# Performance work log

Measured on AMD Instinct MI355X. Metric: run time of the kernel, lower is better.

Reference implementation:

```python
import jax, jax.numpy as jnp
import numpy as np

B, T, C, HS = 4, 2048, 1024, 128

def setup_inputs() -> dict:
    key = jax.random.key(0)
    k0, k1, k2, k3 = jax.random.split(key, 4)
    scale = 1.0 / np.sqrt(C)
    return {
        "x": jax.random.normal(k0, (B, T, C), dtype=jnp.float32),
        "Wk": jax.random.normal(k1, (C, HS), dtype=jnp.float32) * scale,
        "Wq": jax.random.normal(k2, (C, HS), dtype=jnp.float32) * scale,
        "Wv": jax.random.normal(k3, (C, HS), dtype=jnp.float32) * scale,
    }

def reference(x, Wk, Wq, Wv):
    # k, q, v: [B, T, HS]
    k = jnp.einsum('btc,ch->bth', x, Wk)
    q = jnp.einsum('btc,ch->bth', x, Wq)
    v = jnp.einsum('btc,ch->bth', x, Wv)
    hs = k.shape[-1]
    # full T x T scores (no causal mask in source), scaled by head_size**-0.5
    wei = jnp.einsum('bqh,bkh->bqk', q, k) * (hs ** -0.5)
    wei = jax.nn.softmax(wei, axis=-1)
    # dropout p=0.0 -> identity
    out = jnp.einsum('bqk,bkh->bqh', wei, v)
    return out
```

## Files before the change

### kernel.cpp

```cpp
#include <hip/hip_runtime.h>
#include <hip/hip_bf16.h>

typedef float  f32x4  __attribute__((ext_vector_type(4)));
typedef float  f32x8  __attribute__((ext_vector_type(8)));
typedef float  f32x16 __attribute__((ext_vector_type(16)));
typedef short  s8v    __attribute__((ext_vector_type(8)));
typedef __bf16 b8v    __attribute__((ext_vector_type(8)));
typedef unsigned int u32;
typedef unsigned short ushort;

#define T_DIM  2048
#define C_DIM  1024


typedef const __attribute__((address_space(1))) u32 gu32;
typedef __attribute__((address_space(3))) u32 lu32;

static __device__ __forceinline__ void glds16(const void* g, void* l) {
  __builtin_amdgcn_global_load_lds((gu32*)g, (lu32*)l, 16, 0, 0);
}

static __device__ __forceinline__ b8v ldb8(const ushort* p) {
  return __builtin_bit_cast(b8v, *reinterpret_cast<const s8v*>(p));
}

static __device__ __forceinline__ b8v cvt8(f32x8 v) {
  b8v r;
#pragma unroll
  for (int i = 0; i < 8; ++i) r[i] = (__bf16)v[i];
  return r;
}

static __device__ __forceinline__ ushort bfu(float f) {
  __bf16 h = (__bf16)f;
  return __builtin_bit_cast(ushort, h);
}

static __device__ __forceinline__ f32x4 mfma16(b8v a, b8v b, f32x4 c) {
  return __builtin_amdgcn_mfma_f32_16x16x32_bf16(a, b, c, 0, 0, 0);
}

static __device__ __forceinline__ f32x16 mfma32(b8v a, b8v b, f32x16 c) {
  return __builtin_amdgcn_mfma_f32_32x32x16_bf16(a, b, c, 0, 0, 0);
}

#define BAR_VM(N)                                                        \
  asm volatile("s_waitcnt vmcnt(" #N ") lgkmcnt(0)" ::: "memory");       \
  __builtin_amdgcn_s_barrier();                                          \
  asm volatile("" ::: "memory");

__global__ __launch_bounds__(256) void wconv(const float* __restrict__ Wq,
                                             const float* __restrict__ Wk,
                                             const float* __restrict__ Wv,
                                             ushort* __restrict__ Wt) {
  __shared__ float lds[64][65];
  const int m  = blockIdx.z;
  const int c0 = blockIdx.x * 64;
  const int h0 = blockIdx.y * 64;
  const float* W = (m == 0) ? Wq : (m == 1) ? Wk : Wv;

  const int cl = threadIdx.x >> 4;
  const int h4 = (threadIdx.x & 15) * 4;
#pragma unroll
  for (int i = 0; i < 4; ++i) {
    int c = cl + i * 16;
    float4 v = *reinterpret_cast<const float4*>(W + (c0 + c) * 128 + h0 + h4);
    lds[c][h4] = v.x; lds[c][h4 + 1] = v.y;
    lds[c][h4 + 2] = v.z; lds[c][h4 + 3] = v.w;
  }
  __syncthreads();
  const int hl = threadIdx.x >> 2;
  const int cs = (threadIdx.x & 3) * 16;
  s8v o0, o1;
#pragma unroll
  for (int i = 0; i < 8; ++i) o0[i] = (short)bfu(lds[cs + i][hl]);
#pragma unroll
  for (int i = 0; i < 8; ++i) o1[i] = (short)bfu(lds[cs + 8 + i][hl]);
  ushort* dst = Wt + (m * 128 + h0 + hl) * C_DIM + c0 + cs;
  *reinterpret_cast<s8v*>(dst) = o0;
  *reinterpret_cast<s8v*>(dst + 8) = o1;
}

__global__ __launch_bounds__(256) void proj(const float* __restrict__ x,
                                            const ushort* __restrict__ Wt,
                                            ushort* __restrict__ q,
                                            ushort* __restrict__ k,
                                            ushort* __restrict__ vt) {
  __shared__ __align__(16) ushort Ab[2][32 * 72];
  __shared__ __align__(16) ushort Bb[2][128 * 64];
  __shared__ __align__(16) ushort stage[5120];

  const int t   = threadIdx.x;
  const int w   = t >> 6;
  const int lid = t & 63;
  const int lr  = lid & 15;
  const int g   = lid >> 4;
  const int wr  = w >> 1;
  const int wc  = w & 1;
  const int m   = blockIdx.y;
  const int r0  = blockIdx.x * 32;

  const int arow = t >> 3;
  const int acol = (t & 7) * 8;
  const float* ag = x + (r0 + arow) * C_DIM + acol;

  const int bswz = (((lid & 7) ^ (lid >> 3)) << 4);
  const char* bg = (const char*)(Wt + m * 128 * C_DIM);

  f32x4 acc[4] = {};

#pragma unroll
  for (int j = 0; j < 4; ++j) {
    int h = j * 32 + w * 8 + (lid >> 3);
    glds16(bg + h * 2048 + bswz, (char*)&Bb[0][0] + j * 4096 + w * 1024);
  }
  {
    f32x8 av = *reinterpret_cast<const f32x8*>(ag);
    b8v ac = cvt8(av);
    *reinterpret_cast<s8v*>(&Ab[0][arow * 72 + acol]) =
        __builtin_bit_cast(s8v, ac);
  }
  __syncthreads();

  int cur = 0;
#pragma unroll 1
  for (int i = 0; i < 16; ++i) {
    const int nxt = cur ^ 1;
    f32x8 an;
    if (i < 15) {
      const int kk = (i + 1) * 64;
#pragma unroll
      for (int j = 0; j < 4; ++j) {
        int h = j * 32 + w * 8 + (lid >> 3);
        glds16(bg + h * 2048 + kk * 2 + bswz,
               (char*)&Bb[nxt][0] + j * 4096 + w * 1024);
      }
      an = *reinterpret_cast<const f32x8*>(ag + kk);
    }

#pragma unroll
    for (int kk2 = 0; kk2 < 2; ++kk2) {
      b8v af = ldb8(&Ab[cur][(wr * 16 + lr) * 72 + kk2 * 32 + g * 8]);
#pragma unroll
      for (int cn = 0; cn < 4; ++cn) {
        int h = wc * 64 + cn * 16 + lr;
        int inner = (kk2 * 64 + g * 16) ^ ((h & 7) << 4);
        b8v bf = ldb8(
            (const ushort*)((const char*)&Bb[cur][h * 64] + inner));
        acc[cn] = mfma16(af, bf, acc[cn]);
      }
    }

    if (i < 15) {
      b8v anc = cvt8(an);
      *reinterpret_cast<s8v*>(&Ab[nxt][arow * 72 + acol]) =
          __builtin_bit_cast(s8v, anc);
    }
    __syncthreads();
    cur = nxt;
  }

  if (m < 2) {
#pragma unroll
    for (int cn = 0; cn < 4; ++cn)
#pragma unroll
      for (int j = 0; j < 4; ++j)
        stage[(wr * 16 + 4 * g + j) * 136 + wc * 64 + cn * 16 + lr] =
            bfu(acc[cn][j]);
    __syncthreads();
    ushort* dst = (m == 0) ? q : k;
#pragma unroll
    for (int c = 0; c < 2; ++c) {
      int chunk = c * 256 + t;
      int row = chunk >> 4, col8 = chunk & 15;
      s8v v8 = *reinterpret_cast<const s8v*>(&stage[row * 136 + col8 * 8]);
      *reinterpret_cast<s8v*>(&dst[(r0 + row) * 128 + col8 * 8]) = v8;
    }
  } else {
#pragma unroll
    for (int cn = 0; cn < 4; ++cn)
#pragma unroll
      for (int j = 0; j < 4; ++j)
        stage[(wc * 64 + cn * 16 + lr) * 40 + wr * 16 + 4 * g + j] =
            bfu(acc[cn][j]);
    __syncthreads();
    int b = blockIdx.x >> 6;
    int tbase = (blockIdx.x & 63) * 32;
#pragma unroll
    for (int c = 0; c < 2; ++c) {
      int chunk = c * 256 + t;
      int h = chunk >> 2, t8 = chunk & 3;
      s8v v8 = *reinterpret_cast<const s8v*>(&stage[h * 40 + t8 * 8]);
      *reinterpret_cast<s8v*>(&vt[(b * 128 + h) * T_DIM + tbase + t8 * 8]) = v8;
    }
  }
}

__global__ __launch_bounds__(512) void attn(const ushort* __restrict__ q,
                                            const ushort* __restrict__ k,
                                            const ushort* __restrict__ vt,
                                            float* __restrict__ out,
                                            float* __restrict__ opart,
                                            float* __restrict__ lp0,
                                            float* __restrict__ lp1) {
  extern __shared__ __align__(16) char smem[];

  const int t   = threadIdx.x;
  const int w   = t >> 6;
  const int lid = t & 63;
  const int hi  = lid >> 5;
  const int ln  = lid & 31;
  const int wq  = w >> 2;
  const int wk  = w & 3;
  const int b   = blockIdx.y;
  const int z   = blockIdx.z;
  const int t0  = blockIdx.x * 64;

  const ushort* qp = q + (b * T_DIM + t0 + wq * 32) * 128;
  b8v aq[8];
#pragma unroll
  for (int s = 0; s < 8; ++s)
    aq[s] = ldb8(&qp[ln * 128 + s * 16 + hi * 8]);

  const char* kgb = (const char*)(k + b * T_DIM * 128);
  const char* vgb = (const char*)(vt + b * 128 * T_DIM);
  const int kv_base = z * 1024;

  const int R = wk * 32 + ln;
  int koff[8];
#pragma unroll
  for (int s = 0; s < 8; ++s)
    koff[s] = R * 256 + (((s * 2 + hi) ^ (R & 15)) << 4);
  int voff[4][2];
#pragma unroll
  for (int ht = 0; ht < 4; ++ht)
#pragma unroll
    for (int s = 0; s < 2; ++s) {
      int Hrow = ht * 32 + ln;
      int chunk = wk * 4 + s * 2 + hi;
      voff[ht][s] = 32768 + Hrow * 256 + ((chunk ^ (Hrow & 15)) << 4);
    }

  f32x16 of[4] = {};
  float lsum = 0.0f;
  const float scale = 0.08838834764831845f;

#define ATTN_STAGE(KV0, BUF)                                              \
  _Pragma("unroll") for (int j = 0; j < 4; ++j) {                         \
    int row = w * 16 + j * 4 + (lid >> 4);                                \
    int p_ = (row >> 2) & 7;                                              \
    int pg = (p_ & 4) | ((p_ & 1) << 1) | ((p_ >> 1) & 1);                \
    int srow = (row & ~31) | (pg << 2) | (row & 3);                       \
    glds16(kgb + ((KV0) + srow) * 256 + (((lid & 15) ^ (row & 15)) << 4), \
           smem + (BUF) * 65536 + w * 4096 + j * 1024);                   \
  }                                                                       \
  _Pragma("unroll") for (int j = 0; j < 4; ++j) {                         \
    int h = w * 16 + j * 4 + (lid >> 4);                                  \
    glds16(vgb + h * 4096 + (KV0) * 2 + (((lid & 15) ^ (h & 15)) << 4),   \
           smem + (BUF) * 65536 + 32768 + w * 4096 + j * 1024);           \
  }

#define ATTN_BODY(BUF)                                                   \
  {                                                                      \
    const char* Tb = smem + (BUF) * 65536;                               \
    b8v kfr[8];                                                          \
    _Pragma("unroll") for (int s = 0; s < 8; ++s)                        \
        kfr[s] = ldb8((const ushort*)(Tb + koff[s]));                    \
    f32x16 S = {};                                                       \
    __builtin_amdgcn_s_setprio(1);                                       \
    _Pragma("unroll") for (int s = 0; s < 8; ++s)                        \
        S = mfma32(kfr[s], aq[s], S);                                    \
    __builtin_amdgcn_s_setprio(0);                                       \
    float p[16];                                                         \
    _Pragma("unroll") for (int r = 0; r < 16; ++r) {                     \
      p[r] = __expf(S[r] * scale - 4.0f);                                \
      lsum += p[r];                                                      \
    }                                                                    \
    b8v pk0, pk1;                                                        \
    _Pragma("unroll") for (int r = 0; r < 8; ++r) {                      \
      pk0[r] = (__bf16)p[r];                                             \
      pk1[r] = (__bf16)p[8 + r];                                         \
    }                                                                    \
    __builtin_amdgcn_s_setprio(1);                                       \
    _Pragma("unroll") for (int ht = 0; ht < 4; ++ht) {                   \
      b8v v0 = ldb8((const ushort*)(Tb + voff[ht][0]));                  \
      b8v v1 = ldb8((const ushort*)(Tb + voff[ht][1]));                  \
      of[ht] = mfma32(pk0, v0, of[ht]);                                  \
      of[ht] = mfma32(pk1, v1, of[ht]);                                  \
    }                                                                    \
    __builtin_amdgcn_s_setprio(0);                                       \
  }

  ATTN_STAGE(kv_base, 0)

#pragma unroll 1
  for (int i = 0; i < 8; ++i) {
    BAR_VM(0)
    if (i < 7) { ATTN_STAGE(kv_base + (i + 1) * 128, (i + 1) & 1) }
    ATTN_BODY(i & 1)
  }

#undef ATTN_STAGE
#undef ATTN_BODY

  lsum += __shfl_xor(lsum, 32);

  __syncthreads();

  float* ob = (float*)smem;
  float* lb = (float*)(smem + 98304);

  if (lid < 32) lb[(wq * 4 + wk) * 32 + lid] = lsum;
  if (wk != 0) {
#pragma unroll
    for (int ht = 0; ht < 4; ++ht)
#pragma unroll
      for (int r = 0; r < 16; ++r) {
        int qm = (r & 3) + 8 * (r >> 2) + 4 * hi;
        ob[((wk - 1) * 64 + wq * 32 + qm) * 128 + ht * 32 + ln] = of[ht][r];
      }
  }
  __syncthreads();
  if (wk == 0) {
    float* dsto = (z == 0) ? out : opart;
#pragma unroll
    for (int ht = 0; ht < 4; ++ht)
#pragma unroll
      for (int r = 0; r < 16; ++r) {
        int qm = (r & 3) + 8 * (r >> 2) + 4 * hi;
        int row = wq * 32 + qm;
        int col = ht * 32 + ln;
        float val = of[ht][r] + ob[(0 * 64 + row) * 128 + col] +
                    ob[(1 * 64 + row) * 128 + col] +
                    ob[(2 * 64 + row) * 128 + col];
        dsto[(b * T_DIM + t0 + row) * 128 + col] = val;
      }
    if (lid < 32) {
      float lt = lb[(wq * 4 + 0) * 32 + lid] + lb[(wq * 4 + 1) * 32 + lid] +
                 lb[(wq * 4 + 2) * 32 + lid] + lb[(wq * 4 + 3) * 32 + lid];
      float* lp = (z == 0) ? lp0 : lp1;
      lp[b * T_DIM + t0 + wq * 32 + lid] = lt;
    }
  }
}

__global__ __launch_bounds__(256) void fin(float* __restrict__ out,
                                           const float* __restrict__ opart,
                                           const float* __restrict__ lp0,
                                           const float* __restrict__ lp1) {
  int tid = blockIdx.x * 256 + threadIdx.x;
  int idx = tid * 4;
  int row = idx >> 7;
  float inv = 1.0f / (lp0[row] + lp1[row]);
  f32x4 a = *reinterpret_cast<const f32x4*>(out + idx);
  f32x4 c = *reinterpret_cast<const f32x4*>(opart + idx);
  f32x4 r;
#pragma unroll
  for (int i = 0; i < 4; ++i) r[i] = (a[i] + c[i]) * inv;
  *reinterpret_cast<f32x4*>(out + idx) = r;
}

extern "C" void kernel_launch(void* const* d_in, const int* in_sizes, int n_in,
                              void* d_out, int out_size, void* d_ws,
                              size_t ws_size, hipStream_t stream) {
  const float* x  = (const float*)d_in[0];
  const float* Wk = (const float*)d_in[1];
  const float* Wq = (const float*)d_in[2];
  const float* Wv = (const float*)d_in[3];
  float* out = (float*)d_out;

  char* ws = (char*)d_ws;
  ushort* Wt  = (ushort*)ws;
  ushort* qb  = (ushort*)(ws + (1u << 20));
  ushort* kb  = (ushort*)(ws + 3u * (1u << 20));
  ushort* vtb = (ushort*)(ws + 5u * (1u << 20));
  float* opart = (float*)(ws + 8u * (1u << 20));
  float* lp0   = (float*)(ws + 12u * (1u << 20));
  float* lp1   = lp0 + 8192;

  (void)hipFuncSetAttribute(reinterpret_cast<const void*>(&attn),
                            hipFuncAttributeMaxDynamicSharedMemorySize, 131072);

  wconv<<<dim3(16, 2, 3), dim3(256), 0, stream>>>(Wq, Wk, Wv, Wt);
  proj<<<dim3(256, 3), dim3(256), 0, stream>>>(x, Wt, qb, kb, vtb);
  attn<<<dim3(32, 4, 2), dim3(512), 131072, stream>>>(qb, kb, vtb, out, opart,
                                                      lp0, lp1);
  fin<<<dim3(1024), dim3(256), 0, stream>>>(out, opart, lp0, lp1);
}
```

Before: 48.83 us.

## Enlarge projection row tile to 64 and switch to 32x32x16 MFMA

The projection kernel now handles 64 rows of x per block instead of 32, halving the grid and reusing each staged weight tile across twice as many rows. The inner product moves from 16x16x32 to 32x32x16 bf16 MFMAs, with two interleaved accumulators per column tile that are summed at the end, and s_setprio is raised around the MFMA bursts. The epilogue staging is redone for the new accumulator layout. This cuts weight-tile reloads and LDS reads per FLOP, at the cost of fewer blocks (384) and more registers and LDS per block.

Result: slower. 51.90 us (+6.3%).

```diff
diff --git a/kernel.cpp b/kernel.cpp
--- a/kernel.cpp
+++ b/kernel.cpp
@@ -34,10 +34,6 @@
 static __device__ __forceinline__ ushort bfu(float f) {
   __bf16 h = (__bf16)f;
   return __builtin_bit_cast(ushort, h);
-}
-
-static __device__ __forceinline__ f32x4 mfma16(b8v a, b8v b, f32x4 c) {
-  return __builtin_amdgcn_mfma_f32_16x16x32_bf16(a, b, c, 0, 0, 0);
 }
 
 static __device__ __forceinline__ f32x16 mfma32(b8v a, b8v b, f32x16 c) {
@@ -86,39 +82,45 @@
                                             ushort* __restrict__ q,
                                             ushort* __restrict__ k,
                                             ushort* __restrict__ vt) {
-  __shared__ __align__(16) ushort Ab[2][32 * 72];
+  __shared__ __align__(16) ushort Ab[2][64 * 72];
   __shared__ __align__(16) ushort Bb[2][128 * 64];
-  __shared__ __align__(16) ushort stage[5120];
+  __shared__ __align__(16) ushort stage[128 * 72];
 
   const int t   = threadIdx.x;
   const int w   = t >> 6;
   const int lid = t & 63;
-  const int lr  = lid & 15;
-  const int g   = lid >> 4;
-  const int wr  = w >> 1;
-  const int wc  = w & 1;
+  const int hi  = lid >> 5;
+  const int ln  = lid & 31;
+  const int mr  = w >> 1;
+  const int nc  = w & 1;
   const int m   = blockIdx.y;
-  const int r0  = blockIdx.x * 32;
-
-  const int arow = t >> 3;
-  const int acol = (t & 7) * 8;
+  const int r0  = blockIdx.x * 64;
+
+  const int arow = t >> 2;
+  const int acol = (t & 3) * 16;
   const float* ag = x + (r0 + arow) * C_DIM + acol;
 
   const int bswz = (((lid & 7) ^ (lid >> 3)) << 4);
   const char* bg = (const char*)(Wt + m * 128 * C_DIM);
 
-  f32x4 acc[4] = {};
-
-#pragma unroll
-  for (int j = 0; j < 4; ++j) {
-    int h = j * 32 + w * 8 + (lid >> 3);
-    glds16(bg + h * 2048 + bswz, (char*)&Bb[0][0] + j * 4096 + w * 1024);
-  }
+  f32x16 acc[2][2] = {};
+
+#define PROJ_BSTAGE(KK, BUF)                                              \
+  _Pragma("unroll") for (int j = 0; j < 4; ++j) {                         \
+    int h = j * 32 + w * 8 + (lid >> 3);                                  \
+    glds16(bg + h * 2048 + (KK) * 2 + bswz,                               \
+           (char*)&Bb[BUF][0] + j * 4096 + w * 1024);                     \
+  }
+
+  f32x8 a0 = *reinterpret_cast<const f32x8*>(ag);
+  f32x8 a1 = *reinterpret_cast<const f32x8*>(ag + 8);
+  PROJ_BSTAGE(0, 0)
   {
-    f32x8 av = *reinterpret_cast<const f32x8*>(ag);
-    b8v ac = cvt8(av);
+    b8v c0 = cvt8(a0), c1 = cvt8(a1);
     *reinterpret_cast<s8v*>(&Ab[0][arow * 72 + acol]) =
-        __builtin_bit_cast(s8v, ac);
+        __builtin_bit_cast(s8v, c0);
+    *reinterpret_cast<s8v*>(&Ab[0][arow * 72 + acol + 8]) =
+        __builtin_bit_cast(s8v, c1);
   }
   __syncthreads();
 
@@ -126,51 +128,57 @@
 #pragma unroll 1
   for (int i = 0; i < 16; ++i) {
     const int nxt = cur ^ 1;
-    f32x8 an;
     if (i < 15) {
       const int kk = (i + 1) * 64;
-#pragma unroll
-      for (int j = 0; j < 4; ++j) {
-        int h = j * 32 + w * 8 + (lid >> 3);
-        glds16(bg + h * 2048 + kk * 2 + bswz,
-               (char*)&Bb[nxt][0] + j * 4096 + w * 1024);
-      }
-      an = *reinterpret_cast<const f32x8*>(ag + kk);
-    }
-
-#pragma unroll
-    for (int kk2 = 0; kk2 < 2; ++kk2) {
-      b8v af = ldb8(&Ab[cur][(wr * 16 + lr) * 72 + kk2 * 32 + g * 8]);
-#pragma unroll
-      for (int cn = 0; cn < 4; ++cn) {
-        int h = wc * 64 + cn * 16 + lr;
-        int inner = (kk2 * 64 + g * 16) ^ ((h & 7) << 4);
+      PROJ_BSTAGE(kk, nxt)
+      a0 = *reinterpret_cast<const f32x8*>(ag + kk);
+      a1 = *reinterpret_cast<const f32x8*>(ag + kk + 8);
+    }
+
+#pragma unroll
+    for (int s = 0; s < 4; ++s) {
+      b8v af = ldb8(&Ab[cur][(mr * 32 + ln) * 72 + s * 16 + hi * 8]);
+      __builtin_amdgcn_s_setprio(1);
+#pragma unroll
+      for (int ct = 0; ct < 2; ++ct) {
+        int h = nc * 64 + ct * 32 + ln;
+        int inner = ((s * 2 + hi) << 4) ^ ((h & 7) << 4);
         b8v bf = ldb8(
             (const ushort*)((const char*)&Bb[cur][h * 64] + inner));
-        acc[cn] = mfma16(af, bf, acc[cn]);
-      }
+        acc[ct][s & 1] = mfma32(af, bf, acc[ct][s & 1]);
+      }
+      __builtin_amdgcn_s_setprio(0);
     }
 
     if (i < 15) {
-      b8v anc = cvt8(an);
+      b8v c0 = cvt8(a0), c1 = cvt8(a1);
       *reinterpret_cast<s8v*>(&Ab[nxt][arow * 72 + acol]) =
-          __builtin_bit_cast(s8v, anc);
+          __builtin_bit_cast(s8v, c0);
+      *reinterpret_cast<s8v*>(&Ab[nxt][arow * 72 + acol + 8]) =
+          __builtin_bit_cast(s8v, c1);
     }
     __syncthreads();
     cur = nxt;
   }
+#undef PROJ_BSTAGE
+
+  f32x16 fa[2];
+#pragma unroll
+  for (int ct = 0; ct < 2; ++ct) fa[ct] = acc[ct][0] + acc[ct][1];
 
   if (m < 2) {
 #pragma unroll
-    for (int cn = 0; cn < 4; ++cn)
-#pragma unroll
-      for (int j = 0; j < 4; ++j)
-        stage[(wr * 16 + 4 * g + j) * 136 + wc * 64 + cn * 16 + lr] =
-            bfu(acc[cn][j]);
+    for (int ct = 0; ct < 2; ++ct)
+#pragma unroll
+      for (int r = 0; r < 16; ++r) {
+        int row = mr * 32 + (r & 3) + 8 * (r >> 2) + 4 * hi;
+        int col = nc * 64 + ct * 32 + ln;
+        stage[row * 136 + col] = bfu(fa[ct][r]);
+      }
     __syncthreads();
     ushort* dst = (m == 0) ? q : k;
 #pragma unroll
-    for (int c = 0; c < 2; ++c) {
+    for (int c = 0; c < 4; ++c) {
       int chunk = c * 256 + t;
       int row = chunk >> 4, col8 = chunk & 15;
       s8v v8 = *reinterpret_cast<const s8v*>(&stage[row * 136 + col8 * 8]);
@@ -178,20 +186,22 @@
     }
   } else {
 #pragma unroll
-    for (int cn = 0; cn < 4; ++cn)
-#pragma unroll
-      for (int j = 0; j < 4; ++j)
-        stage[(wc * 64 + cn * 16 + lr) * 40 + wr * 16 + 4 * g + j] =
-            bfu(acc[cn][j]);
+    for (int ct = 0; ct < 2; ++ct)
+#pragma unroll
+      for (int r = 0; r < 16; ++r) {
+        int trow = mr * 32 + (r & 3) + 8 * (r >> 2) + 4 * hi;
+        int h = nc * 64 + ct * 32 + ln;
+        stage[h * 72 + trow] = bfu(fa[ct][r]);
+      }
     __syncthreads();
-    int b = blockIdx.x >> 6;
-    int tbase = (blockIdx.x & 63) * 32;
-#pragma unroll
-    for (int c = 0; c < 2; ++c) {
+    int bb = blockIdx.x >> 5;
+    int tbase = (blockIdx.x & 31) * 64;
+#pragma unroll
+    for (int c = 0; c < 4; ++c) {
       int chunk = c * 256 + t;
-      int h = chunk >> 2, t8 = chunk & 3;
-      s8v v8 = *reinterpret_cast<const s8v*>(&stage[h * 40 + t8 * 8]);
-      *reinterpret_cast<s8v*>(&vt[(b * 128 + h) * T_DIM + tbase + t8 * 8]) = v8;
+      int h = chunk >> 3, t8 = chunk & 7;
+      s8v v8 = *reinterpret_cast<const s8v*>(&stage[h * 72 + t8 * 8]);
+      *reinterpret_cast<s8v*>(&vt[(bb * 128 + h) * T_DIM + tbase + t8 * 8]) = v8;
     }
   }
 }
@@ -382,7 +392,7 @@
                             hipFuncAttributeMaxDynamicSharedMemorySize, 131072);
 
   wconv<<<dim3(16, 2, 3), dim3(256), 0, stream>>>(Wq, Wk, Wv, Wt);
-  proj<<<dim3(256, 3), dim3(256), 0, stream>>>(x, Wt, qb, kb, vtb);
+  proj<<<dim3(128, 3), dim3(256), 0, stream>>>(x, Wt, qb, kb, vtb);
   attn<<<dim3(32, 4, 2), dim3(512), 131072, stream>>>(qb, kb, vtb, out, opart,
                                                       lp0, lp1);
   fin<<<dim3(1024), dim3(256), 0, stream>>>(out, opart, lp0, lp1);
```

## Add 4-way KV split attention kernel with 128-query tiles when workspace allows

Applied to the files above, without the earlier changes.

Adds an attn4 kernel that processes 128 query rows per block, using 8 waves arranged as 4 query groups by 2 KV halves. Each staged K/V tile is reused across twice as many queries, and the KV sequence is split 4 ways (grid 16x4x4), which keeps 256 blocks. The finalize kernel is generalized to sum nz partial outputs and row sums. This path is selected only when the workspace is at least 21 MiB; otherwise the original 2-way kernel runs. The cost is more partial-output traffic in the finalize step and a dependence on the workspace size.

Result: no change. 48.87 us (+0.1%).

```diff
diff --git a/kernel.cpp b/kernel.cpp
--- a/kernel.cpp
+++ b/kernel.cpp
@@ -195,55 +195,6 @@
     }
   }
 }
-
-__global__ __launch_bounds__(512) void attn(const ushort* __restrict__ q,
-                                            const ushort* __restrict__ k,
-                                            const ushort* __restrict__ vt,
-                                            float* __restrict__ out,
-                                            float* __restrict__ opart,
-                                            float* __restrict__ lp0,
-                                            float* __restrict__ lp1) {
-  extern __shared__ __align__(16) char smem[];
-
-  const int t   = threadIdx.x;
-  const int w   = t >> 6;
-  const int lid = t & 63;
-  const int hi  = lid >> 5;
-  const int ln  = lid & 31;
-  const int wq  = w >> 2;
-  const int wk  = w & 3;
-  const int b   = blockIdx.y;
-  const int z   = blockIdx.z;
-  const int t0  = blockIdx.x * 64;
-
-  const ushort* qp = q + (b * T_DIM + t0 + wq * 32) * 128;
-  b8v aq[8];
-#pragma unroll
-  for (int s = 0; s < 8; ++s)
-    aq[s] = ldb8(&qp[ln * 128 + s * 16 + hi * 8]);
-
-  const char* kgb = (const char*)(k + b * T_DIM * 128);
-  const char* vgb = (const char*)(vt + b * 128 * T_DIM);
-  const int kv_base = z * 1024;
-
-  const int R = wk * 32 + ln;
-  int koff[8];
-#pragma unroll
-  for (int s = 0; s < 8; ++s)
-    koff[s] = R * 256 + (((s * 2 + hi) ^ (R & 15)) << 4);
-  int voff[4][2];
-#pragma unroll
-  for (int ht = 0; ht < 4; ++ht)
-#pragma unroll
-    for (int s = 0; s < 2; ++s) {
-      int Hrow = ht * 32 + ln;
-      int chunk = wk * 4 + s * 2 + hi;
-      voff[ht][s] = 32768 + Hrow * 256 + ((chunk ^ (Hrow & 15)) << 4);
-    }
-
-  f32x16 of[4] = {};
-  float lsum = 0.0f;
-  const float scale = 0.08838834764831845f;
 
 #define ATTN_STAGE(KV0, BUF)                                              \
   _Pragma("unroll") for (int j = 0; j < 4; ++j) {                         \
@@ -260,7 +211,55 @@
            smem + (BUF) * 65536 + 32768 + w * 4096 + j * 1024);           \
   }
 
-#define ATTN_BODY(BUF)                                                   \
+__global__ __launch_bounds__(512) void attn2(const ushort* __restrict__ q,
+                                             const ushort* __restrict__ k,
+                                             const ushort* __restrict__ vt,
+                                             float* __restrict__ out,
+                                             float* __restrict__ parts,
+                                             float* __restrict__ lps) {
+  extern __shared__ __align__(16) char smem[];
+
+  const int t   = threadIdx.x;
+  const int w   = t >> 6;
+  const int lid = t & 63;
+  const int hi  = lid >> 5;
+  const int ln  = lid & 31;
+  const int wq  = w >> 2;
+  const int wk  = w & 3;
+  const int b   = blockIdx.y;
+  const int z   = blockIdx.z;
+  const int t0  = blockIdx.x * 64;
+
+  const ushort* qp = q + (b * T_DIM + t0 + wq * 32) * 128;
+  b8v aq[8];
+#pragma unroll
+  for (int s = 0; s < 8; ++s)
+    aq[s] = ldb8(&qp[ln * 128 + s * 16 + hi * 8]);
+
+  const char* kgb = (const char*)(k + b * T_DIM * 128);
+  const char* vgb = (const char*)(vt + b * 128 * T_DIM);
+  const int kv_base = z * 1024;
+
+  const int R = wk * 32 + ln;
+  int koff[8];
+#pragma unroll
+  for (int s = 0; s < 8; ++s)
+    koff[s] = R * 256 + (((s * 2 + hi) ^ (R & 15)) << 4);
+  int voff[4][2];
+#pragma unroll
+  for (int ht = 0; ht < 4; ++ht)
+#pragma unroll
+    for (int s = 0; s < 2; ++s) {
+      int Hrow = ht * 32 + ln;
+      int chunk = wk * 4 + s * 2 + hi;
+      voff[ht][s] = 32768 + Hrow * 256 + ((chunk ^ (Hrow & 15)) << 4);
+    }
+
+  f32x16 of[4] = {};
+  float lsum = 0.0f;
+  const float scale = 0.08838834764831845f;
+
+#define ATTN2_BODY(BUF)                                                  \
   {                                                                      \
     const char* Tb = smem + (BUF) * 65536;                               \
     b8v kfr[8];                                                          \
@@ -297,11 +296,9 @@
   for (int i = 0; i < 8; ++i) {
     BAR_VM(0)
     if (i < 7) { ATTN_STAGE(kv_base + (i + 1) * 128, (i + 1) & 1) }
-    ATTN_BODY(i & 1)
-  }
-
-#undef ATTN_STAGE
-#undef ATTN_BODY
+    ATTN2_BODY(i & 1)
+  }
+#undef ATTN2_BODY
 
   lsum += __shfl_xor(lsum, 32);
 
@@ -322,7 +319,7 @@
   }
   __syncthreads();
   if (wk == 0) {
-    float* dsto = (z == 0) ? out : opart;
+    float* dsto = (z == 0) ? out : parts;
 #pragma unroll
     for (int ht = 0; ht < 4; ++ht)
 #pragma unroll
@@ -338,25 +335,161 @@
     if (lid < 32) {
       float lt = lb[(wq * 4 + 0) * 32 + lid] + lb[(wq * 4 + 1) * 32 + lid] +
                  lb[(wq * 4 + 2) * 32 + lid] + lb[(wq * 4 + 3) * 32 + lid];
-      float* lp = (z == 0) ? lp0 : lp1;
-      lp[b * T_DIM + t0 + wq * 32 + lid] = lt;
+      lps[z * 8192 + b * T_DIM + t0 + wq * 32 + lid] = lt;
+    }
+  }
+}
+
+__global__ __launch_bounds__(512) void attn4(const ushort* __restrict__ q,
+                                             const ushort* __restrict__ k,
+                                             const ushort* __restrict__ vt,
+                                             float* __restrict__ out,
+                                             float* __restrict__ parts,
+                                             float* __restrict__ lps) {
+  extern __shared__ __align__(16) char smem[];
+
+  const int t   = threadIdx.x;
+  const int w   = t >> 6;
+  const int lid = t & 63;
+  const int hi  = lid >> 5;
+  const int ln  = lid & 31;
+  const int wq  = w >> 1;
+  const int wk  = w & 1;
+  const int b   = blockIdx.y;
+  const int z   = blockIdx.z;
+  const int t0  = blockIdx.x * 128;
+
+  const ushort* qp = q + (b * T_DIM + t0 + wq * 32) * 128;
+  b8v aq[8];
+#pragma unroll
+  for (int s = 0; s < 8; ++s)
+    aq[s] = ldb8(&qp[ln * 128 + s * 16 + hi * 8]);
+
+  const char* kgb = (const char*)(k + b * T_DIM * 128);
+  const char* vgb = (const char*)(vt + b * 128 * T_DIM);
+  const int kv_base = z * 512;
+
+  int koff[2][8];
+#pragma unroll
+  for (int tt = 0; tt < 2; ++tt) {
+    int R = wk * 64 + tt * 32 + ln;
+#pragma unroll
+    for (int s = 0; s < 8; ++s)
+      koff[tt][s] = R * 256 + (((s * 2 + hi) ^ (R & 15)) << 4);
+  }
+  int voff[2][4][2];
+#pragma unroll
+  for (int tt = 0; tt < 2; ++tt)
+#pragma unroll
+    for (int ht = 0; ht < 4; ++ht)
+#pragma unroll
+      for (int s = 0; s < 2; ++s) {
+        int Hrow = ht * 32 + ln;
+        int chunk = wk * 8 + tt * 4 + s * 2 + hi;
+        voff[tt][ht][s] = 32768 + Hrow * 256 + ((chunk ^ (Hrow & 15)) << 4);
+      }
+
+  f32x16 of[4] = {};
+  float lsum = 0.0f;
+  const float scale = 0.08838834764831845f;
+
+#define ATTN4_HALF(TB, TT)                                               \
+  {                                                                      \
+    b8v kfr[8];                                                          \
+    _Pragma("unroll") for (int s = 0; s < 8; ++s)                        \
+        kfr[s] = ldb8((const ushort*)((TB) + koff[TT][s]));              \
+    f32x16 S = {};                                                       \
+    __builtin_amdgcn_s_setprio(1);                                       \
+    _Pragma("unroll") for (int s = 0; s < 8; ++s)                        \
+        S = mfma32(kfr[s], aq[s], S);                                    \
+    __builtin_amdgcn_s_setprio(0);                                       \
+    float p[16];                                                         \
+    _Pragma("unroll") for (int r = 0; r < 16; ++r) {                     \
+      p[r] = __expf(S[r] * scale - 4.0f);                                \
+      lsum += p[r];                                                      \
+    }                                                                    \
+    b8v pk0, pk1;                                                        \
+    _Pragma("unroll") for (int r = 0; r < 8; ++r) {                      \
+      pk0[r] = (__bf16)p[r];                                             \
+      pk1[r] = (__bf16)p[8 + r];                                         \
+    }                                                                    \
+    __builtin_amdgcn_s_setprio(1);                                       \
+    _Pragma("unroll") for (int ht = 0; ht < 4; ++ht) {                   \
+      b8v v0 = ldb8((const ushort*)((TB) + voff[TT][ht][0]));            \
+      b8v v1 = ldb8((const ushort*)((TB) + voff[TT][ht][1]));            \
+      of[ht] = mfma32(pk0, v0, of[ht]);                                  \
+      of[ht] = mfma32(pk1, v1, of[ht]);                                  \
+    }                                                                    \
+    __builtin_amdgcn_s_setprio(0);                                       \
+  }
+
+  ATTN_STAGE(kv_base, 0)
+
+#pragma unroll 1
+  for (int i = 0; i < 4; ++i) {
+    BAR_VM(0)
+    if (i < 3) { ATTN_STAGE(kv_base + (i + 1) * 128, (i + 1) & 1) }
+    const char* Tb = smem + (i & 1) * 65536;
+    ATTN4_HALF(Tb, 0)
+    ATTN4_HALF(Tb, 1)
+  }
+#undef ATTN4_HALF
+
+  lsum += __shfl_xor(lsum, 32);
+
+  __syncthreads();
+
+  float* ob = (float*)smem;
+  float* lb = (float*)(smem + 65536);
+
+  if (lid < 32) lb[(wk * 4 + wq) * 32 + lid] = lsum;
+  if (wk == 1) {
+#pragma unroll
+    for (int ht = 0; ht < 4; ++ht)
+#pragma unroll
+      for (int r = 0; r < 16; ++r) {
+        int qm = (r & 3) + 8 * (r >> 2) + 4 * hi;
+        ob[(wq * 32 + qm) * 128 + ht * 32 + ln] = of[ht][r];
+      }
+  }
+  __syncthreads();
+  if (wk == 0) {
+    float* dsto = (z == 0) ? out : (parts + (z - 1) * 1048576);
+#pragma unroll
+    for (int ht = 0; ht < 4; ++ht)
+#pragma unroll
+      for (int r = 0; r < 16; ++r) {
+        int qm = (r & 3) + 8 * (r >> 2) + 4 * hi;
+        int row = wq * 32 + qm;
+        int col = ht * 32 + ln;
+        float val = of[ht][r] + ob[row * 128 + col];
+        dsto[(b * T_DIM + t0 + row) * 128 + col] = val;
+      }
+    if (lid < 32) {
+      float lt = lb[(0 * 4 + wq) * 32 + lid] + lb[(1 * 4 + wq) * 32 + lid];
+      lps[z * 8192 + b * T_DIM + t0 + wq * 32 + lid] = lt;
     }
   }
 }
 
 __global__ __launch_bounds__(256) void fin(float* __restrict__ out,
-                                           const float* __restrict__ opart,
-                                           const float* __restrict__ lp0,
-                                           const float* __restrict__ lp1) {
+                                           const float* __restrict__ parts,
+                                           const float* __restrict__ lps,
+                                           int nz) {
   int tid = blockIdx.x * 256 + threadIdx.x;
   int idx = tid * 4;
   int row = idx >> 7;
-  float inv = 1.0f / (lp0[row] + lp1[row]);
+  float l = lps[row];
+  for (int zz = 1; zz < nz; ++zz) l += lps[zz * 8192 + row];
+  float inv = 1.0f / l;
   f32x4 a = *reinterpret_cast<const f32x4*>(out + idx);
-  f32x4 c = *reinterpret_cast<const f32x4*>(opart + idx);
+  for (int zz = 1; zz < nz; ++zz) {
+    f32x4 c = *reinterpret_cast<const f32x4*>(parts + (zz - 1) * 1048576 + idx);
+    a += c;
+  }
   f32x4 r;
 #pragma unroll
-  for (int i = 0; i < 4; ++i) r[i] = (a[i] + c[i]) * inv;
+  for (int i = 0; i < 4; ++i) r[i] = a[i] * inv;
   *reinterpret_cast<f32x4*>(out + idx) = r;
 }
 
@@ -374,16 +507,26 @@
   ushort* qb  = (ushort*)(ws + (1u << 20));
   ushort* kb  = (ushort*)(ws + 3u * (1u << 20));
   ushort* vtb = (ushort*)(ws + 5u * (1u << 20));
-  float* opart = (float*)(ws + 8u * (1u << 20));
-  float* lp0   = (float*)(ws + 12u * (1u << 20));
-  float* lp1   = lp0 + 8192;
-
-  (void)hipFuncSetAttribute(reinterpret_cast<const void*>(&attn),
+  float* parts = (float*)(ws + 8u * (1u << 20));
+
+  const bool big = ws_size >= (21u << 20);
+  float* lps = big ? (float*)(ws + 20u * (1u << 20))
+                   : (float*)(ws + 12u * (1u << 20));
+
+  (void)hipFuncSetAttribute(reinterpret_cast<const void*>(&attn2),
+                            hipFuncAttributeMaxDynamicSharedMemorySize, 131072);
+  (void)hipFuncSetAttribute(reinterpret_cast<const void*>(&attn4),
                             hipFuncAttributeMaxDynamicSharedMemorySize, 131072);
 
   wconv<<<dim3(16, 2, 3), dim3(256), 0, stream>>>(Wq, Wk, Wv, Wt);
   proj<<<dim3(256, 3), dim3(256), 0, stream>>>(x, Wt, qb, kb, vtb);
-  attn<<<dim3(32, 4, 2), dim3(512), 131072, stream>>>(qb, kb, vtb, out, opart,
-                                                      lp0, lp1);
-  fin<<<dim3(1024), dim3(256), 0, stream>>>(out, opart, lp0, lp1);
-}
+  if (big) {
+    attn4<<<dim3(16, 4, 4), dim3(512), 131072, stream>>>(qb, kb, vtb, out,
+                                                         parts, lps);
+    fin<<<dim3(1024), dim3(256), 0, stream>>>(out, parts, lps, 4);
+  } else {
+    attn2<<<dim3(32, 4, 2), dim3(512), 131072, stream>>>(qb, kb, vtb, out,
+                                                         parts, lps);
+    fin<<<dim3(1024), dim3(256), 0, stream>>>(out, parts, lps, 2);
+  }
+}
```
